# Optimization experiments

Measured on AMD Instinct MI355X. Metric: run time of the kernel, lower is better.

Reference implementation:

```python
import jax, jax.numpy as jnp
import numpy as np

B, T, C = 4, 2048, 1024


def setup_inputs() -> dict:
    key = jax.random.key(0)
    ks = jax.random.split(key, 7)
    s = 1.0 / np.sqrt(C)
    return {
        "x": jax.random.normal(ks[0], (B, T, C), dtype=jnp.float32),
        "Wq": jax.random.normal(ks[1], (C, C), dtype=jnp.float32) * s,
        "bq": jnp.zeros((C,), dtype=jnp.float32),
        "Wk": jax.random.normal(ks[2], (C, C), dtype=jnp.float32) * s,
        "bk": jnp.zeros((C,), dtype=jnp.float32),
        "Wv": jax.random.normal(ks[3], (C, C), dtype=jnp.float32) * s,
        "bv": jnp.zeros((C,), dtype=jnp.float32),
    }


def reference(x, Wq, bq, Wk, bk, Wv, bv):
    # q/k/v projections (torch Linear: x @ W^T + b; here W stored as [C_in, C_out])
    q = x @ Wq + bq  # (B, T, C)
    k = x @ Wk + bk
    v = x @ Wv + bv
    scale = 1.0 / jnp.sqrt(jnp.asarray(C, dtype=x.dtype))
    att = jnp.einsum("btc,bsc->bts", q, k) * scale  # (B, T, T)
    # causal mask: additive -inf above the diagonal
    causal = jnp.tril(jnp.ones((T, T), dtype=bool))
    att = jnp.where(causal, att, jnp.asarray(-jnp.inf, dtype=att.dtype))
    att = jax.nn.softmax(att, axis=-1)
    # dropout is identity in eval/reference mode
    out = jnp.einsum("bts,bsc->btc", att, v)  # (B, T, C)
    return out
```

## Files before the change

### kernel.cpp

```cpp
#include <hip/hip_runtime.h>

#define B_ 4
#define T_ 2048
#define C_ 1024

typedef unsigned short u16;
typedef unsigned int u32;
typedef short sh8 __attribute__((ext_vector_type(8)));
typedef float f32x4 __attribute__((ext_vector_type(4)));

__device__ __forceinline__ float bf2f(u16 u) {
    union { float f; u32 i; } c; c.i = ((u32)u) << 16; return c.f;
}
__device__ __forceinline__ u16 f2bf(float f) {
    union { float f; u32 i; } c; c.f = f;
    return (u16)((c.i + 0x7FFFu + ((c.i >> 16) & 1u)) >> 16);
}

__device__ __forceinline__ void gload_lds16(const void* g, void* l) {
    __builtin_amdgcn_global_load_lds(
        (const __attribute__((address_space(1))) u32*)g,
        (__attribute__((address_space(3))) u32*)l, 16, 0, 0);
}

__device__ __forceinline__ void wait_vm8()   { asm volatile("s_waitcnt vmcnt(8)" ::: "memory"); }
__device__ __forceinline__ void wait_vm4()   { asm volatile("s_waitcnt vmcnt(4)" ::: "memory"); }
__device__ __forceinline__ void wait_vm0()   { asm volatile("s_waitcnt vmcnt(0)" ::: "memory"); }
__device__ __forceinline__ void barrier_raw(){ asm volatile("s_barrier" ::: "memory"); }

template<bool RS>
__device__ __forceinline__ void mm_core(
    const u16* __restrict__ A, const u16* __restrict__ B,
    int ldA, int ldB, int nk64,
    u16* lds, f32x4 (&acc)[4][4], f32x4* rsacc, int tid)
{
    const int w  = tid >> 6, l = tid & 63;
    const int fr = l & 15,  fq = l >> 4;
    const int wm = (w & 1) << 6, wn = (w >> 1) << 6;
    const int rl = l >> 3;
    const int pc = l & 7;
    const int cg = pc ^ rl;

    sh8 ones;
    if (RS) {
#pragma unroll
        for (int e = 0; e < 8; ++e) ones[e] = (short)0x3F80;
    }

    auto issue = [&](int kt) {
        const int ko = kt << 6;
        u16* dA = lds + ((kt & 1) << 14);
        u16* dB = dA + 8192;
#pragma unroll
        for (int t = 0; t < 4; ++t) {
            const int r0 = w * 32 + t * 8;
            const int r  = r0 + rl;
            gload_lds16(A + (size_t)r * ldA + ko + cg * 8, dA + ((size_t)r0 * 8 + l) * 8);
            gload_lds16(B + (size_t)r * ldB + ko + cg * 8, dB + ((size_t)r0 * 8 + l) * 8);
        }
    };

    issue(0);
    issue(1);

    for (int kt = 0; kt < nk64; ++kt) {
        if (kt + 1 < nk64) wait_vm8(); else wait_vm0();
        barrier_raw();
        u16* bufA = lds + ((kt & 1) << 14);
        u16* bufB = bufA + 8192;
#pragma unroll
        for (int kk = 0; kk < 2; ++kk) {
            sh8 af[4], bf[4];
            const int g = kk * 4 + fq;
#pragma unroll
            for (int i = 0; i < 4; ++i) {
                const int m = wm + i * 16 + fr;
                af[i] = *(const sh8*)(bufA + ((size_t)m * 8 + (g ^ (m & 7))) * 8);
                const int n = wn + i * 16 + fr;
                bf[i] = *(const sh8*)(bufB + ((size_t)n * 8 + (g ^ (n & 7))) * 8);
            }
#pragma unroll
            for (int i = 0; i < 4; ++i) {
#pragma unroll
                for (int j = 0; j < 4; ++j)
                    acc[i][j] = __builtin_amdgcn_mfma_f32_16x16x32_bf16(af[i], bf[j], acc[i][j], 0, 0, 0);
                if (RS)
                    rsacc[i] = __builtin_amdgcn_mfma_f32_16x16x32_bf16(af[i], ones, rsacc[i], 0, 0, 0);
            }
        }
        barrier_raw();
        if (kt + 2 < nk64) issue(kt + 2);
    }
}

__global__ __launch_bounds__(256) void cvt_all(
    const float* __restrict__ x,
    const float* __restrict__ Wq, const float* __restrict__ Wk, const float* __restrict__ Wv,
    u16* __restrict__ xb, u16* __restrict__ wt)
{
    __shared__ float tile[64][68];
    const int bid = blockIdx.x;
    if (bid < 8192) {
        size_t i = ((size_t)bid * 256 + threadIdx.x) * 4;
        float4 f = *(const float4*)(x + i);
        ushort4 o;
        o.x = f2bf(f.x); o.y = f2bf(f.y); o.z = f2bf(f.z); o.w = f2bf(f.w);
        *(ushort4*)(xb + i) = o;
        return;
    }
    const int r = bid - 8192;
    const int z = r >> 8;
    const int rr = r & 255;
    const int n0 = (rr & 15) * 64, k0 = (rr >> 4) * 64;
    const float* W = z == 0 ? Wq : (z == 1 ? Wk : Wv);
    u16* out = wt + (size_t)z * C_ * C_;
    const int tx = threadIdx.x & 15, ty = threadIdx.x >> 4;
#pragma unroll
    for (int rr2 = 0; rr2 < 4; ++rr2) {
        int row = ty + rr2 * 16;
        *(float4*)&tile[row][tx * 4] = *(const float4*)(W + (size_t)(k0 + row) * C_ + n0 + tx * 4);
    }
    __syncthreads();
#pragma unroll
    for (int rr2 = 0; rr2 < 4; ++rr2) {
        int n = ty + rr2 * 16;
        ushort4 o;
        o.x = f2bf(tile[tx * 4 + 0][n]);
        o.y = f2bf(tile[tx * 4 + 1][n]);
        o.z = f2bf(tile[tx * 4 + 2][n]);
        o.w = f2bf(tile[tx * 4 + 3][n]);
        *(ushort4*)(out + (size_t)(n0 + n) * C_ + k0 + tx * 4) = o;
    }
}

__global__ __launch_bounds__(512, 2) void qkv8(
    const u16* __restrict__ xb, const u16* __restrict__ wt,
    const float* __restrict__ bq, const float* __restrict__ bk, const float* __restrict__ bv,
    u16* __restrict__ qo, u16* __restrict__ ko, u16* __restrict__ vto)
{
    __shared__ __align__(16) u16 smem[65536];
    const int bid = blockIdx.x;
    const int wg  = (bid & 7) * 48 + (bid >> 3);
    const int z   = wg >> 7;
    const int tt  = wg & 127;
    const int n0  = (tt >> 5) << 8;
    const int m0  = (tt & 31) << 8;
    const int tid = threadIdx.x;

    const u16* Ag = xb + (size_t)m0 * C_;
    const u16* Bg = wt + (size_t)z * C_ * C_ + (size_t)n0 * C_;

    const int l  = tid & 63, w = tid >> 6;
    const int fr = l & 15,  fq = l >> 4;
    const int wm = (w >> 2) << 7;
    const int wn = (w & 3) << 6;

    const int srow = tid >> 2, spg = tid & 3;
    const int slg  = spg ^ ((srow >> 1) & 3);
    const u16* aS0 = Ag + (size_t)srow * C_ + slg * 8;
    const u16* aS1 = Ag + (size_t)(srow + 128) * C_ + slg * 8;
    const u16* bS0 = Bg + (size_t)srow * C_ + slg * 8;
    const u16* bS1 = Bg + (size_t)(srow + 128) * C_ + slg * 8;

    auto stageA = [&](int sl) {
        u16* d = smem + ((sl & 3) << 14);
        gload_lds16(aS0 + sl * 32, d + tid * 8);
        gload_lds16(aS1 + sl * 32, d + 4096 + tid * 8);
    };
    auto stageB = [&](int sl) {
        u16* d = smem + ((sl & 3) << 14) + 8192;
        gload_lds16(bS0 + sl * 32, d + tid * 8);
        gload_lds16(bS1 + sl * 32, d + 4096 + tid * 8);
    };

    f32x4 acc[8][4];
#pragma unroll
    for (int i = 0; i < 8; ++i)
#pragma unroll
        for (int j = 0; j < 4; ++j) acc[i][j] = 0.0f;

    stageA(0); stageB(0);
    stageA(1); stageB(1);
    stageA(2); stageB(2);
    wait_vm8();
    barrier_raw();

#pragma unroll 4
    for (int sk = 0; sk < 32; ++sk) {
        const u16* bA = smem + ((sk & 3) << 14);
        const u16* bB = bA + 8192;
        sh8 af[8], bf[2];
#pragma unroll
        for (int i = 0; i < 8; ++i) {
            const int m = wm + i * 16 + fr;
            af[i] = *(const sh8*)(bA + ((m << 2) + (fq ^ ((m >> 1) & 3))) * 8);
        }
#pragma unroll
        for (int jj = 0; jj < 2; ++jj) {
            const int n = wn + jj * 16 + fr;
            bf[jj] = *(const sh8*)(bB + ((n << 2) + (fq ^ ((n >> 1) & 3))) * 8);
        }
        if (sk + 3 < 32) stageA(sk + 3);
        barrier_raw();
        __builtin_amdgcn_s_setprio(1);
#pragma unroll
        for (int i = 0; i < 8; ++i) {
            acc[i][0] = __builtin_amdgcn_mfma_f32_16x16x32_bf16(af[i], bf[0], acc[i][0], 0, 0, 0);
            acc[i][1] = __builtin_amdgcn_mfma_f32_16x16x32_bf16(af[i], bf[1], acc[i][1], 0, 0, 0);
        }
        __builtin_amdgcn_s_setprio(0);
        barrier_raw();
#pragma unroll
        for (int jj = 0; jj < 2; ++jj) {
            const int n = wn + (2 + jj) * 16 + fr;
            bf[jj] = *(const sh8*)(bB + ((n << 2) + (fq ^ ((n >> 1) & 3))) * 8);
        }
        if (sk + 3 < 32) stageB(sk + 3);
        barrier_raw();
        __builtin_amdgcn_s_setprio(1);
#pragma unroll
        for (int i = 0; i < 8; ++i) {
            acc[i][2] = __builtin_amdgcn_mfma_f32_16x16x32_bf16(af[i], bf[0], acc[i][2], 0, 0, 0);
            acc[i][3] = __builtin_amdgcn_mfma_f32_16x16x32_bf16(af[i], bf[1], acc[i][3], 0, 0, 0);
        }
        __builtin_amdgcn_s_setprio(0);
        if      (sk + 3 < 32) wait_vm8();
        else if (sk + 2 < 32) wait_vm4();
        else if (sk + 1 < 32) wait_vm0();
        barrier_raw();
    }

    const float* bias = z == 0 ? bq : (z == 1 ? bk : bv);
#pragma unroll
    for (int j = 0; j < 4; ++j) {
        const int col = wn + j * 16 + fr;
        const float bb = bias[n0 + col];
        const int cg = col >> 3, ce = col & 7;
#pragma unroll
        for (int i = 0; i < 8; ++i)
#pragma unroll
            for (int r = 0; r < 4; ++r) {
                const int row = wm + i * 16 + fq * 4 + r;
                smem[row * 256 + ((cg ^ ((row >> 3) & 31)) << 3) + ce] = f2bf(acc[i][j][r] + bb);
            }
    }
    __syncthreads();

    if (z < 2) {
        u16* out = z == 0 ? qo : ko;
#pragma unroll
        for (int p = 0; p < 16; ++p) {
            const int idx = p * 512 + tid;
            const int row = idx >> 5;
            const int c16 = idx & 31;
            uint4 v = *(const uint4*)&smem[row * 256 + ((c16 ^ ((row >> 3) & 31)) << 3)];
            *(uint4*)(out + (size_t)(m0 + row) * C_ + n0 + c16 * 8) = v;
        }
    } else {
        const int b  = m0 >> 11;
        const int t0 = m0 & 2047;
        u16* vt = vto + (size_t)b * C_ * T_;
#pragma unroll
        for (int p = 0; p < 16; ++p) {
            const int idx = p * 512 + tid;
            const int cl = idx >> 5;
            const int ch = idx & 31;
            const int cg = cl >> 3, ce = cl & 7;
            u16 tmp[8];
#pragma unroll
            for (int e = 0; e < 8; ++e) {
                const int row = ch * 8 + e;
                tmp[e] = smem[row * 256 + ((cg ^ ((row >> 3) & 31)) << 3) + ce];
            }
            *(uint4*)(vt + (size_t)(n0 + cl) * T_ + t0 + ch * 8) = *(uint4*)tmp;
        }
    }
}

__device__ __constant__ size_t att_off[4] = {
    0, (size_t)1 << 22, (size_t)1 << 25, ((size_t)1 << 25) + ((size_t)1 << 22)
};

__global__ __launch_bounds__(256, 2) void scores_mfma(
    const u16* __restrict__ qb, const u16* __restrict__ kb, u16* __restrict__ wsbase)
{
    int t = blockIdx.x;
    int by = (int)((sqrtf(8.f * t + 1.f) - 1.f) * 0.5f);
    while ((by + 1) * (by + 2) / 2 <= t) ++by;
    while (by * (by + 1) / 2 > t) --by;
    const int bx = t - by * (by + 1) / 2;
    const int b = blockIdx.z;
    const int s0 = bx * 128, m0 = by * 128;
    __shared__ __align__(16) u16 smem[32768];
    const u16* Q = qb + (size_t)b * T_ * C_ + (size_t)m0 * C_;
    const u16* K = kb + (size_t)b * T_ * C_ + (size_t)s0 * C_;
    const int tid = threadIdx.x;
    f32x4 acc[4][4];
#pragma unroll
    for (int i = 0; i < 4; ++i)
#pragma unroll
        for (int j = 0; j < 4; ++j) acc[i][j] = 0.0f;

    mm_core<false>(Q, K, C_, C_, C_ / 64, smem, acc, nullptr, tid);

    const int w = tid >> 6, l = tid & 63, fr = l & 15, fq = l >> 4;
    const int wm = (w & 1) << 6, wn = (w >> 1) << 6;
#pragma unroll
    for (int i = 0; i < 4; ++i)
#pragma unroll
        for (int r = 0; r < 4; ++r) {
            const int lm = wm + i * 16 + fq * 4 + r;
            const int m = m0 + lm;
#pragma unroll
            for (int j = 0; j < 4; ++j) {
                const int ls = wn + j * 16 + fr;
                const int s = s0 + ls;
                float e = (s <= m) ? __expf(acc[i][j][r] * 0.03125f) : 0.f;
                smem[lm * 136 + ls] = f2bf(e);
            }
        }
    __syncthreads();
    u16* att = wsbase + att_off[b] + (size_t)m0 * T_ + s0;
    const int rr = tid >> 4, cc = tid & 15;
#pragma unroll
    for (int p = 0; p < 8; ++p) {
        const int row = p * 16 + rr;
        uint4 val = *(const uint4*)&smem[row * 136 + cc * 8];
        *(uint4*)(att + (size_t)row * T_ + cc * 8) = val;
    }
}

__global__ __launch_bounds__(256, 2) void pv_mfma(
    const u16* __restrict__ wsbase, const u16* __restrict__ vt,
    float* __restrict__ outp)
{
    const int b = blockIdx.z;
    const int n0 = blockIdx.x * 128;
    const int by = 15 - blockIdx.y;
    const int m0 = by * 128;
    __shared__ __align__(16) u16 smem[32768];
    const u16* A  = wsbase + att_off[b] + (size_t)m0 * T_;
    const u16* Bp = vt + (size_t)b * C_ * T_ + (size_t)n0 * T_;
    const int tid = threadIdx.x;
    f32x4 acc[4][4], rs[4];
#pragma unroll
    for (int i = 0; i < 4; ++i) {
        rs[i] = 0.0f;
#pragma unroll
        for (int j = 0; j < 4; ++j) acc[i][j] = 0.0f;
    }

    mm_core<true>(A, Bp, T_, T_, (m0 + 128) >> 6, smem, acc, rs, tid);

    const int w = tid >> 6, l = tid & 63, fr = l & 15, fq = l >> 4;
    const int wm = (w & 1) << 6, wn = (w >> 1) << 6;
    float* fb = (float*)smem;
#pragma unroll
    for (int p = 0; p < 2; ++p) {
        if ((w & 1) == p) {
#pragma unroll
            for (int i = 0; i < 4; ++i)
#pragma unroll
                for (int r = 0; r < 4; ++r) {
                    const int rr2 = i * 16 + fq * 4 + r;
                    const float inv = 1.0f / rs[i][r];
#pragma unroll
                    for (int j = 0; j < 4; ++j)
                        fb[rr2 * 132 + wn + j * 16 + fr] = acc[i][j][r] * inv;
                }
        }
        __syncthreads();
        const int rr = tid >> 5, cc = (tid & 31) * 4;
#pragma unroll
        for (int k2 = 0; k2 < 8; ++k2) {
            const int row = k2 * 8 + rr;
            float4 val = *(const float4*)&fb[row * 132 + cc];
            *(float4*)(outp + ((size_t)b * T_ + m0 + p * 64 + row) * C_ + n0 + cc) = val;
        }
        __syncthreads();
    }
}

extern "C" void kernel_launch(void* const* d_in, const int* in_sizes, int n_in,
                              void* d_out, int out_size, void* d_ws, size_t ws_size,
                              hipStream_t stream) {
    const float* x  = (const float*)d_in[0];
    const float* Wq = (const float*)d_in[1];
    const float* bq = (const float*)d_in[2];
    const float* Wk = (const float*)d_in[3];
    const float* bk = (const float*)d_in[4];
    const float* Wv = (const float*)d_in[5];
    const float* bv = (const float*)d_in[6];
    float* out = (float*)d_out;

    char* ws = (char*)d_ws;
    u16* xb   = (u16*)ws;
    u16* q    = (u16*)(ws + (16ull << 20));
    u16* k    = (u16*)(ws + (32ull << 20));
    u16* vt   = (u16*)(ws + (48ull << 20));
    u16* wt   = (u16*)(ws + (64ull << 20));
    u16* attb = (u16*)ws;

    cvt_all <<<8960, 256, 0, stream>>>(x, Wq, Wk, Wv, xb, wt);
    qkv8    <<<384, 512, 0, stream>>>(xb, wt, bq, bk, bv, q, k, vt);
    scores_mfma<<<dim3(136, 1, 4), 256, 0, stream>>>(q, k, attb);
    pv_mfma    <<<dim3(8, 16, 4), 256, 0, stream>>>(attb, vt, out);
}
```

Before: 248.1 us.

## Retile QKV projection GEMM to 128x192 tiles over fused 3C output

Replaces the 256x256, 512-thread QKV GEMM with a 128x192 tile, 256-thread kernel that treats Wq/Wk/Wv as one fused 3072-wide output, launching 1024 workgroups instead of 384. This aims to fix wave quantization and improve CU occupancy across the GPU, at the cost of lower per-tile data reuse. Tiles can straddle q/k/v boundaries, so the epilogue now picks bias and destination per column and writes V transposed through an unswizzled padded LDS buffer, which may cause bank conflicts.

```diff
diff --git a/kernel.cpp b/kernel.cpp
--- a/kernel.cpp
+++ b/kernel.cpp
@@ -23,8 +23,9 @@
         (__attribute__((address_space(3))) u32*)l, 16, 0, 0);
 }
 
+__device__ __forceinline__ void wait_vm10()  { asm volatile("s_waitcnt vmcnt(10)" ::: "memory"); }
 __device__ __forceinline__ void wait_vm8()   { asm volatile("s_waitcnt vmcnt(8)" ::: "memory"); }
-__device__ __forceinline__ void wait_vm4()   { asm volatile("s_waitcnt vmcnt(4)" ::: "memory"); }
+__device__ __forceinline__ void wait_vm5()   { asm volatile("s_waitcnt vmcnt(5)" ::: "memory"); }
 __device__ __forceinline__ void wait_vm0()   { asm volatile("s_waitcnt vmcnt(0)" ::: "memory"); }
 __device__ __forceinline__ void barrier_raw(){ asm volatile("s_barrier" ::: "memory"); }
 
@@ -133,146 +134,160 @@
     }
 }
 
-__global__ __launch_bounds__(512, 2) void qkv8(
+__global__ __launch_bounds__(256, 2) void qkv_p(
     const u16* __restrict__ xb, const u16* __restrict__ wt,
     const float* __restrict__ bq, const float* __restrict__ bk, const float* __restrict__ bv,
     u16* __restrict__ qo, u16* __restrict__ ko, u16* __restrict__ vto)
 {
-    __shared__ __align__(16) u16 smem[65536];
+    __shared__ __align__(16) u16 smem[40960];
     const int bid = blockIdx.x;
-    const int wg  = (bid & 7) * 48 + (bid >> 3);
-    const int z   = wg >> 7;
-    const int tt  = wg & 127;
-    const int n0  = (tt >> 5) << 8;
-    const int m0  = (tt & 31) << 8;
+    const int wg  = (bid & 7) * 128 + (bid >> 3);
+    const int mt  = wg >> 4;
+    const int nt  = wg & 15;
+    const int m0  = mt << 7;
+    const int n0  = nt * 192;
     const int tid = threadIdx.x;
 
     const u16* Ag = xb + (size_t)m0 * C_;
-    const u16* Bg = wt + (size_t)z * C_ * C_ + (size_t)n0 * C_;
+    const u16* Bg = wt + (size_t)n0 * C_;
 
     const int l  = tid & 63, w = tid >> 6;
     const int fr = l & 15,  fq = l >> 4;
-    const int wm = (w >> 2) << 7;
-    const int wn = (w & 3) << 6;
+    const int wm = (w & 1) << 6;
+    const int wn = (w >> 1) * 96;
 
     const int srow = tid >> 2, spg = tid & 3;
-    const int slg  = spg ^ ((srow >> 1) & 3);
-    const u16* aS0 = Ag + (size_t)srow * C_ + slg * 8;
-    const u16* aS1 = Ag + (size_t)(srow + 128) * C_ + slg * 8;
-    const u16* bS0 = Bg + (size_t)srow * C_ + slg * 8;
-    const u16* bS1 = Bg + (size_t)(srow + 128) * C_ + slg * 8;
+    const int rA0 = srow,      rA1 = srow + 64;
+    const int rB0 = srow,      rB1 = srow + 64, rB2 = srow + 128;
+    const int lgA0 = spg ^ ((rA0 >> 1) & 3), lgA1 = spg ^ ((rA1 >> 1) & 3);
+    const int lgB0 = lgA0, lgB1 = lgA1, lgB2 = spg ^ ((rB2 >> 1) & 3);
+    const u16* aS0 = Ag + (size_t)rA0 * C_ + lgA0 * 8;
+    const u16* aS1 = Ag + (size_t)rA1 * C_ + lgA1 * 8;
+    const u16* bS0 = Bg + (size_t)rB0 * C_ + lgB0 * 8;
+    const u16* bS1 = Bg + (size_t)rB1 * C_ + lgB1 * 8;
+    const u16* bS2 = Bg + (size_t)rB2 * C_ + lgB2 * 8;
 
     auto stageA = [&](int sl) {
-        u16* d = smem + ((sl & 3) << 14);
+        u16* d = smem + (size_t)(sl & 3) * 10240;
         gload_lds16(aS0 + sl * 32, d + tid * 8);
-        gload_lds16(aS1 + sl * 32, d + 4096 + tid * 8);
+        gload_lds16(aS1 + sl * 32, d + 2048 + tid * 8);
     };
     auto stageB = [&](int sl) {
-        u16* d = smem + ((sl & 3) << 14) + 8192;
+        u16* d = smem + (size_t)(sl & 3) * 10240 + 4096;
         gload_lds16(bS0 + sl * 32, d + tid * 8);
-        gload_lds16(bS1 + sl * 32, d + 4096 + tid * 8);
+        gload_lds16(bS1 + sl * 32, d + 2048 + tid * 8);
+        gload_lds16(bS2 + sl * 32, d + 4096 + tid * 8);
     };
 
-    f32x4 acc[8][4];
-#pragma unroll
-    for (int i = 0; i < 8; ++i)
-#pragma unroll
-        for (int j = 0; j < 4; ++j) acc[i][j] = 0.0f;
+    f32x4 acc[4][6];
+#pragma unroll
+    for (int i = 0; i < 4; ++i)
+#pragma unroll
+        for (int j = 0; j < 6; ++j) acc[i][j] = 0.0f;
 
     stageA(0); stageB(0);
     stageA(1); stageB(1);
     stageA(2); stageB(2);
-    wait_vm8();
+    wait_vm10();
     barrier_raw();
 
 #pragma unroll 4
     for (int sk = 0; sk < 32; ++sk) {
-        const u16* bA = smem + ((sk & 3) << 14);
-        const u16* bB = bA + 8192;
-        sh8 af[8], bf[2];
-#pragma unroll
-        for (int i = 0; i < 8; ++i) {
+        const u16* sA = smem + (size_t)(sk & 3) * 10240;
+        const u16* sB = sA + 4096;
+        sh8 af[4], bf[3];
+#pragma unroll
+        for (int i = 0; i < 4; ++i) {
             const int m = wm + i * 16 + fr;
-            af[i] = *(const sh8*)(bA + ((m << 2) + (fq ^ ((m >> 1) & 3))) * 8);
-        }
-#pragma unroll
-        for (int jj = 0; jj < 2; ++jj) {
+            af[i] = *(const sh8*)(sA + ((m << 2) + (fq ^ ((m >> 1) & 3))) * 8);
+        }
+#pragma unroll
+        for (int jj = 0; jj < 3; ++jj) {
             const int n = wn + jj * 16 + fr;
-            bf[jj] = *(const sh8*)(bB + ((n << 2) + (fq ^ ((n >> 1) & 3))) * 8);
+            bf[jj] = *(const sh8*)(sB + ((n << 2) + (fq ^ ((n >> 1) & 3))) * 8);
         }
         if (sk + 3 < 32) stageA(sk + 3);
         barrier_raw();
         __builtin_amdgcn_s_setprio(1);
 #pragma unroll
-        for (int i = 0; i < 8; ++i) {
+        for (int i = 0; i < 4; ++i) {
             acc[i][0] = __builtin_amdgcn_mfma_f32_16x16x32_bf16(af[i], bf[0], acc[i][0], 0, 0, 0);
             acc[i][1] = __builtin_amdgcn_mfma_f32_16x16x32_bf16(af[i], bf[1], acc[i][1], 0, 0, 0);
+            acc[i][2] = __builtin_amdgcn_mfma_f32_16x16x32_bf16(af[i], bf[2], acc[i][2], 0, 0, 0);
         }
         __builtin_amdgcn_s_setprio(0);
         barrier_raw();
 #pragma unroll
-        for (int jj = 0; jj < 2; ++jj) {
-            const int n = wn + (2 + jj) * 16 + fr;
-            bf[jj] = *(const sh8*)(bB + ((n << 2) + (fq ^ ((n >> 1) & 3))) * 8);
+        for (int jj = 0; jj < 3; ++jj) {
+            const int n = wn + (3 + jj) * 16 + fr;
+            bf[jj] = *(const sh8*)(sB + ((n << 2) + (fq ^ ((n >> 1) & 3))) * 8);
         }
         if (sk + 3 < 32) stageB(sk + 3);
         barrier_raw();
         __builtin_amdgcn_s_setprio(1);
 #pragma unroll
-        for (int i = 0; i < 8; ++i) {
-            acc[i][2] = __builtin_amdgcn_mfma_f32_16x16x32_bf16(af[i], bf[0], acc[i][2], 0, 0, 0);
-            acc[i][3] = __builtin_amdgcn_mfma_f32_16x16x32_bf16(af[i], bf[1], acc[i][3], 0, 0, 0);
+        for (int i = 0; i < 4; ++i) {
+            acc[i][3] = __builtin_amdgcn_mfma_f32_16x16x32_bf16(af[i], bf[0], acc[i][3], 0, 0, 0);
+            acc[i][4] = __builtin_amdgcn_mfma_f32_16x16x32_bf16(af[i], bf[1], acc[i][4], 0, 0, 0);
+            acc[i][5] = __builtin_amdgcn_mfma_f32_16x16x32_bf16(af[i], bf[2], acc[i][5], 0, 0, 0);
         }
         __builtin_amdgcn_s_setprio(0);
-        if      (sk + 3 < 32) wait_vm8();
-        else if (sk + 2 < 32) wait_vm4();
-        else if (sk + 1 < 32) wait_vm0();
-        barrier_raw();
-    }
-
-    const float* bias = z == 0 ? bq : (z == 1 ? bk : bv);
-#pragma unroll
-    for (int j = 0; j < 4; ++j) {
+        if      (sk < 29) wait_vm10();
+        else if (sk == 29) wait_vm5();
+        else if (sk == 30) wait_vm0();
+        barrier_raw();
+    }
+
+    u16* bb = smem;
+#pragma unroll
+    for (int j = 0; j < 6; ++j) {
         const int col = wn + j * 16 + fr;
-        const float bb = bias[n0 + col];
-        const int cg = col >> 3, ce = col & 7;
-#pragma unroll
-        for (int i = 0; i < 8; ++i)
+        const int gc  = n0 + col;
+        const int z   = gc >> 10;
+        const int cw  = gc & 1023;
+        const float bv_ = (z == 0 ? bq : (z == 1 ? bk : bv))[cw];
+#pragma unroll
+        for (int i = 0; i < 4; ++i)
 #pragma unroll
             for (int r = 0; r < 4; ++r) {
                 const int row = wm + i * 16 + fq * 4 + r;
-                smem[row * 256 + ((cg ^ ((row >> 3) & 31)) << 3) + ce] = f2bf(acc[i][j][r] + bb);
+                bb[row * 200 + col] = f2bf(acc[i][j][r] + bv_);
             }
     }
     __syncthreads();
 
-    if (z < 2) {
-        u16* out = z == 0 ? qo : ko;
-#pragma unroll
-        for (int p = 0; p < 16; ++p) {
-            const int idx = p * 512 + tid;
-            const int row = idx >> 5;
-            const int c16 = idx & 31;
-            uint4 v = *(const uint4*)&smem[row * 256 + ((c16 ^ ((row >> 3) & 31)) << 3)];
-            *(uint4*)(out + (size_t)(m0 + row) * C_ + n0 + c16 * 8) = v;
-        }
-    } else {
-        const int b  = m0 >> 11;
-        const int t0 = m0 & 2047;
-        u16* vt = vto + (size_t)b * C_ * T_;
-#pragma unroll
-        for (int p = 0; p < 16; ++p) {
-            const int idx = p * 512 + tid;
-            const int cl = idx >> 5;
-            const int ch = idx & 31;
-            const int cg = cl >> 3, ce = cl & 7;
-            u16 tmp[8];
-#pragma unroll
-            for (int e = 0; e < 8; ++e) {
-                const int row = ch * 8 + e;
-                tmp[e] = smem[row * 256 + ((cg ^ ((row >> 3) & 31)) << 3) + ce];
-            }
-            *(uint4*)(vt + (size_t)(n0 + cl) * T_ + t0 + ch * 8) = *(uint4*)tmp;
+    {
+        const int r    = tid >> 1;
+        const int half = tid & 1;
+#pragma unroll
+        for (int q = 0; q < 12; ++q) {
+            const int c8  = half * 12 + q;
+            const int gc0 = n0 + c8 * 8;
+            const int z   = gc0 >> 10;
+            if (z < 2) {
+                uint4 v = *(const uint4*)&bb[r * 200 + c8 * 8];
+                u16* out = z == 0 ? qo : ko;
+                *(uint4*)(out + (size_t)(m0 + r) * C_ + (gc0 & 1023)) = v;
+            }
+        }
+    }
+    {
+        const int bidx = m0 >> 11;
+        const int t0   = m0 & 2047;
+        u16* vt = vto + (size_t)bidx * C_ * T_;
+#pragma unroll
+        for (int g = 0; g < 12; ++g) {
+            const int gc0 = n0 + g * 16;
+            if (gc0 >= 2048) {
+                const int col   = g * 16 + (tid >> 4);
+                const int chunk = tid & 15;
+                const int c     = (n0 + col) - 2048;
+                u16 tmp[8];
+#pragma unroll
+                for (int e = 0; e < 8; ++e)
+                    tmp[e] = bb[(chunk * 8 + e) * 200 + col];
+                *(uint4*)(vt + (size_t)c * T_ + t0 + chunk * 8) = *(uint4*)tmp;
+            }
         }
     }
 }
@@ -402,7 +417,7 @@
     u16* attb = (u16*)ws;
 
     cvt_all <<<8960, 256, 0, stream>>>(x, Wq, Wk, Wv, xb, wt);
-    qkv8    <<<384, 512, 0, stream>>>(xb, wt, bq, bk, bv, q, k, vt);
+    qkv_p   <<<1024, 256, 0, stream>>>(xb, wt, bq, bk, bv, q, k, vt);
     scores_mfma<<<dim3(136, 1, 4), 256, 0, stream>>>(q, k, attb);
     pv_mfma    <<<dim3(8, 16, 4), 256, 0, stream>>>(attb, vt, out);
 }
```

Result: no change. 247.2 us (-0.4%).
